# Kernel tuning notes

Measured on AMD Instinct MI355X. Metric: run time of the kernel, lower is better.

Reference implementation:

```python
import jax, jax.numpy as jnp
import numpy as np

B, S, HIDDEN = 2, 2048, 2048
HQ, HKV, D = 16, 4, 128
EPS = 1e-6
SCALE = D ** -0.5


def _deinterleave(x):
    # [..., D] interleaved pairs -> [x0,x2,...,x1,x3,...] (half layout)
    *lead, d = x.shape
    return x.reshape(*lead, d // 2, 2).swapaxes(-1, -2).reshape(*lead, d)


def _interleave(x):
    # inverse of _deinterleave
    *lead, d = x.shape
    return x.reshape(*lead, 2, d // 2).swapaxes(-1, -2).reshape(*lead, d)


def _rotate_half(x):
    x1, x2 = jnp.split(x, 2, axis=-1)
    return jnp.concatenate([-x2, x1], axis=-1)


def _rmsnorm(x, w):
    var = jnp.mean(jnp.square(x), axis=-1, keepdims=True)
    return x * jax.lax.rsqrt(var + EPS) * w


def setup_inputs() -> dict:
    key = jax.random.key(0)
    k0, k1, k2, k3, k4 = jax.random.split(key, 5)
    hidden_states = jax.random.normal(k0, (B, S, HIDDEN), jnp.float32)
    cos = jax.random.uniform(k1, (S, D), jnp.float32, -1.0, 1.0)
    sin = jax.random.uniform(k2, (S, D), jnp.float32, -1.0, 1.0)
    qkv_w = jax.random.normal(k3, ((HQ + 2 * HKV) * D, HIDDEN), jnp.float32) * 0.02
    qk_norm_w = jnp.ones((D,), jnp.float32)
    o_w = jax.random.normal(k4, (HIDDEN, HQ * D), jnp.float32) * 0.02
    return {"hidden_states": hidden_states, "cos": cos, "sin": sin,
            "qkv_w": qkv_w, "qk_norm_w": qk_norm_w, "o_w": o_w}


def reference(hidden_states, cos, sin, qkv_w, qk_norm_w, o_w):
    b, s, _ = hidden_states.shape
    qkv = jnp.einsum('bsh,oh->bso', hidden_states, qkv_w)  # [B,S,(HQ+2HKV)*D]
    q = qkv[..., : HQ * D].reshape(b, s, HQ, D)
    k = qkv[..., HQ * D:(HQ + HKV) * D].reshape(b, s, HKV, D)
    v = qkv[..., (HQ + HKV) * D:].reshape(b, s, HKV, D)

    # interleaved-layout RoPE: deinterleave -> rotate-half RoPE -> re-interleave
    q, k = _deinterleave(q), _deinterleave(k)
    cs = cos[None, :, None, :]
    sn = sin[None, :, None, :]
    q = q * cs + _rotate_half(q) * sn
    k = k * cs + _rotate_half(k) * sn
    q, k = _interleave(q), _interleave(k)

    # QK RMSNorm (shared weight over head_dim)
    q = _rmsnorm(q, qk_norm_w)
    k = _rmsnorm(k, qk_norm_w)

    # causal GQA attention
    g = HQ // HKV
    qg = q.reshape(b, s, HKV, g, D)
    scores = jnp.einsum('bshgd,bthd->bhgst', qg, k) * SCALE  # [B,HKV,g,S,S]
    causal = jnp.tril(jnp.ones((s, s), bool))
    scores = jnp.where(causal, scores, jnp.finfo(scores.dtype).min)
    probs = jax.nn.softmax(scores, axis=-1)
    attn = jnp.einsum('bhgst,bthd->bshgd', probs, v).reshape(b, s, HQ * D)

    return jnp.einsum('bsd,od->bso', attn, o_w)
```

## Files before the change

### kernel.cpp

```cpp
#include <hip/hip_runtime.h>
#include <hip/hip_bf16.h>

typedef __bf16 bf16_t;
typedef bf16_t bf16x8 __attribute__((ext_vector_type(8)));
typedef float f32x4 __attribute__((ext_vector_type(4)));
typedef float f32x16 __attribute__((ext_vector_type(16)));
typedef unsigned short u16;
typedef unsigned int u32;

#define B_    2
#define S_    2048
#define HID   2048
#define NQKV  3072
#define HQ_   16
#define HKV_  4
#define D_    128
#define QSCALE_ 0.12751879526600565f

__device__ __forceinline__ u16 f2b(float f) {
    __hip_bfloat16 h = __float2bfloat16(f);
    return *reinterpret_cast<u16*>(&h);
}

__global__ __launch_bounds__(256) void cvt_f32_bf16(const float* __restrict__ in,
                                                    u16* __restrict__ out, int n4) {
    int i = blockIdx.x * 256 + threadIdx.x;
    if (i >= n4) return;
    float4 v = reinterpret_cast<const float4*>(in)[i];
    ushort4 o;
    o.x = f2b(v.x); o.y = f2b(v.y); o.z = f2b(v.z); o.w = f2b(v.w);
    reinterpret_cast<ushort4*>(out)[i] = o;
}

__global__ __launch_bounds__(512, 1) void gemm256_bt(const u16* __restrict__ A,
                                                     const u16* __restrict__ Bm,
                                                     float* __restrict__ C,
                                                     int M, int N, int K) {
    extern __shared__ __align__(16) char smem[];
    u16* Asm = (u16*)smem;
    u16* Bsm = (u16*)smem + 32768;

    const int tid  = threadIdx.x;
    const int lane = tid & 63;
    const int wid  = tid >> 6;
    const int wr = wid >> 2, wc = wid & 3;
    const int lrow = lane & 15, lgrp = lane >> 4;
    const int swz  = (lrow & 7) << 4;
    const int m0 = blockIdx.x * 256, n0 = blockIdx.y * 256;

    const int stRow = tid >> 3;
    const int stCol = ((((tid & 7) * 16) ^ ((stRow & 7) << 4)) >> 1);

    const u16* aBase = A  + (size_t)(m0 + stRow) * K + stCol;
    const u16* bBase = Bm + (size_t)(n0 + stRow) * K + stCol;

    auto glds = [&](const u16* g, u16* l) {
        __builtin_amdgcn_global_load_lds(
            (const __attribute__((address_space(1))) void*)g,
            (__attribute__((address_space(3))) void*)l, 16, 0, 0);
    };
    auto stageA = [&](int buf, int h, int k0) {
        const u16* g = aBase + (size_t)(128 * h) * K + k0;
        u16* d = Asm + buf * 16384 + (1024 * h + tid) * 8;
        glds(g, d);
        glds(g + (size_t)64 * K, d + 512 * 8);
    };
    auto stageB = [&](int buf, int h, int k0) {
        const u16* g = bBase + (size_t)(128 * h) * K + k0;
        u16* d = Bsm + buf * 16384 + (1024 * h + tid) * 8;
        glds(g, d);
        glds(g + (size_t)64 * K, d + 512 * 8);
    };

    f32x4 acc[8][4] = {};
    const int KT = K >> 6;

    stageA(0, 0, 0); stageA(0, 1, 0); stageB(0, 0, 0); stageB(0, 1, 0);

    for (int x = 0; x < KT; ++x) {
        const int cur = x & 1;
        const int kn  = (x + 1) << 6;
        const bool pf = (x + 1 < KT);
        const char* aT = (const char*)(Asm + cur * 16384);
        const char* bT = (const char*)(Bsm + cur * 16384);

        auto ldA = [&](int mi, int ks) -> bf16x8 {
            int row = wr * 128 + mi * 16 + lrow;
            return *(const bf16x8*)(aT + row * 128 + ((ks * 64 + lgrp * 16) ^ swz));
        };
        auto ldB = [&](int ni, int ks) -> bf16x8 {
            int row = wc * 64 + ni * 16 + lrow;
            return *(const bf16x8*)(bT + row * 128 + ((ks * 64 + lgrp * 16) ^ swz));
        };

        bf16x8 afr[4][2], bfr[2][2];

        if (pf) {
            stageA(cur ^ 1, 0, kn);
            asm volatile("s_waitcnt vmcnt(2)" ::: "memory");
        } else {
            asm volatile("s_waitcnt vmcnt(0)" ::: "memory");
        }
        __builtin_amdgcn_s_barrier();
        #pragma unroll
        for (int mi = 0; mi < 4; ++mi) { afr[mi][0] = ldA(mi, 0); afr[mi][1] = ldA(mi, 1); }
        #pragma unroll
        for (int ni = 0; ni < 2; ++ni) { bfr[ni][0] = ldB(ni, 0); bfr[ni][1] = ldB(ni, 1); }
        __builtin_amdgcn_s_setprio(1);
        #pragma unroll
        for (int mi = 0; mi < 4; ++mi)
            #pragma unroll
            for (int ni = 0; ni < 2; ++ni) {
                acc[mi][ni] = __builtin_amdgcn_mfma_f32_16x16x32_bf16(afr[mi][0], bfr[ni][0], acc[mi][ni], 0, 0, 0);
                acc[mi][ni] = __builtin_amdgcn_mfma_f32_16x16x32_bf16(afr[mi][1], bfr[ni][1], acc[mi][ni], 0, 0, 0);
            }
        __builtin_amdgcn_s_setprio(0);
        __builtin_amdgcn_s_barrier();

        #pragma unroll
        for (int ni = 0; ni < 2; ++ni) { bfr[ni][0] = ldB(ni + 2, 0); bfr[ni][1] = ldB(ni + 2, 1); }
        if (pf) stageA(cur ^ 1, 1, kn);
        __builtin_amdgcn_s_barrier();
        __builtin_amdgcn_s_setprio(1);
        #pragma unroll
        for (int mi = 0; mi < 4; ++mi)
            #pragma unroll
            for (int ni = 0; ni < 2; ++ni) {
                acc[mi][ni + 2] = __builtin_amdgcn_mfma_f32_16x16x32_bf16(afr[mi][0], bfr[ni][0], acc[mi][ni + 2], 0, 0, 0);
                acc[mi][ni + 2] = __builtin_amdgcn_mfma_f32_16x16x32_bf16(afr[mi][1], bfr[ni][1], acc[mi][ni + 2], 0, 0, 0);
            }
        __builtin_amdgcn_s_setprio(0);
        __builtin_amdgcn_s_barrier();

        #pragma unroll
        for (int mi = 0; mi < 4; ++mi) { afr[mi][0] = ldA(mi + 4, 0); afr[mi][1] = ldA(mi + 4, 1); }
        if (pf) stageB(cur ^ 1, 0, kn);
        __builtin_amdgcn_s_barrier();
        __builtin_amdgcn_s_setprio(1);
        #pragma unroll
        for (int mi = 0; mi < 4; ++mi)
            #pragma unroll
            for (int ni = 0; ni < 2; ++ni) {
                acc[mi + 4][ni + 2] = __builtin_amdgcn_mfma_f32_16x16x32_bf16(afr[mi][0], bfr[ni][0], acc[mi + 4][ni + 2], 0, 0, 0);
                acc[mi + 4][ni + 2] = __builtin_amdgcn_mfma_f32_16x16x32_bf16(afr[mi][1], bfr[ni][1], acc[mi + 4][ni + 2], 0, 0, 0);
            }
        __builtin_amdgcn_s_setprio(0);
        __builtin_amdgcn_s_barrier();

        #pragma unroll
        for (int ni = 0; ni < 2; ++ni) { bfr[ni][0] = ldB(ni, 0); bfr[ni][1] = ldB(ni, 1); }
        if (pf) stageB(cur ^ 1, 1, kn);
        __builtin_amdgcn_s_barrier();
        __builtin_amdgcn_s_setprio(1);
        #pragma unroll
        for (int mi = 0; mi < 4; ++mi)
            #pragma unroll
            for (int ni = 0; ni < 2; ++ni) {
                acc[mi + 4][ni] = __builtin_amdgcn_mfma_f32_16x16x32_bf16(afr[mi][0], bfr[ni][0], acc[mi + 4][ni], 0, 0, 0);
                acc[mi + 4][ni] = __builtin_amdgcn_mfma_f32_16x16x32_bf16(afr[mi][1], bfr[ni][1], acc[mi + 4][ni], 0, 0, 0);
            }
        __builtin_amdgcn_s_setprio(0);
        __builtin_amdgcn_s_barrier();
    }

    #pragma unroll
    for (int mi = 0; mi < 8; ++mi)
        #pragma unroll
        for (int ni = 0; ni < 4; ++ni) {
            int r = m0 + wr * 128 + mi * 16 + lgrp * 4;
            int c = n0 + wc * 64 + ni * 16 + lrow;
            float* p = C + (size_t)r * N + c;
            #pragma unroll
            for (int i = 0; i < 4; ++i) p[(size_t)i * N] = acc[mi][ni][i];
        }
}

__global__ __launch_bounds__(256) void rope_norm_split(const float* __restrict__ qkv,
                                                       const float* __restrict__ cosb,
                                                       const float* __restrict__ sinb,
                                                       const float* __restrict__ nw,
                                                       u16* __restrict__ qb,
                                                       u16* __restrict__ kb,
                                                       u16* __restrict__ vb) {
    const int row  = blockIdx.x;
    const int b    = row >> 11;
    const int s    = row & 2047;
    const int wave = threadIdx.x >> 6;
    const int lane = threadIdx.x & 63;
    const float* base = qkv + (size_t)row * NQKV;

    const float c0 = cosb[s * 128 + lane];
    const float c1 = cosb[s * 128 + 64 + lane];
    const float s0 = sinb[s * 128 + lane];
    const float s1 = sinb[s * 128 + 64 + lane];
    const float w0 = nw[2 * lane];
    const float w1 = nw[2 * lane + 1];

    for (int h = wave; h < HQ_ + HKV_; h += 4) {
        float2 x = *(const float2*)(base + h * 128 + 2 * lane);
        float y0 = x.x * c0 - x.y * s0;
        float y1 = x.y * c1 + x.x * s1;
        float ss = y0 * y0 + y1 * y1;
        #pragma unroll
        for (int off = 32; off; off >>= 1) ss += __shfl_xor(ss, off);
        float r = rsqrtf(ss * (1.0f / 128.0f) + 1e-6f);
        float o0 = y0 * r * w0, o1 = y1 * r * w1;
        if (h < HQ_) {
            u32 pack = (u32)f2b(o0 * QSCALE_) | ((u32)f2b(o1 * QSCALE_) << 16);
            *(u32*)(qb + ((size_t)(b * HQ_ + h) * S_ + s) * D_ + 2 * lane) = pack;
        } else {
            u32 pack = (u32)f2b(o0) | ((u32)f2b(o1) << 16);
            *(u32*)(kb + ((size_t)(b * HKV_ + (h - HQ_)) * S_ + s) * D_ + 2 * lane) = pack;
        }
    }
    {
        int h = wave;
        float2 x = *(const float2*)(base + (HQ_ + HKV_) * 128 + h * 128 + 2 * lane);
        u32 pack = (u32)f2b(x.x) | ((u32)f2b(x.y) << 16);
        *(u32*)(vb + ((size_t)(b * HKV_ + h) * S_ + s) * D_ + 2 * lane) = pack;
    }
}

__global__ __launch_bounds__(256) void transpose_v(const u16* __restrict__ vb,
                                                   u16* __restrict__ vtb) {
    __shared__ u16 t[64][72];
    const int s0 = blockIdx.x * 64, d0 = blockIdx.y * 64, bh = blockIdx.z;
    const u16* src = vb  + (size_t)bh * S_ * D_;
    u16*       dst = vtb + (size_t)bh * D_ * S_;
    const int tid = threadIdx.x;

    {
        int r = tid >> 3, c8 = (tid & 7) * 8;
        #pragma unroll
        for (int p = 0; p < 2; p++) {
            int rr = r + p * 32;
            *(uint4*)&t[rr][c8] = *(const uint4*)(src + (size_t)(s0 + rr) * D_ + d0 + c8);
        }
    }
    __syncthreads();
    {
        int dd = tid & 63;
        int sb = (tid >> 6) * 8;
        #pragma unroll
        for (int p = 0; p < 2; p++) {
            int ss8 = sb + p * 32;
            union { u16 u[8]; uint4 v; } pk;
            #pragma unroll
            for (int j = 0; j < 8; j++) pk.u[j] = t[ss8 + j][dd];
            *(uint4*)(dst + (size_t)(d0 + dd) * S_ + s0 + ss8) = pk.v;
        }
    }
}

__global__ __launch_bounds__(256, 2) void attn_fwd3(const u16* __restrict__ qb,
                                                    const u16* __restrict__ kb,
                                                    const u16* __restrict__ vtb,
                                                    u16* __restrict__ attn) {
    __shared__ __align__(16) u16 Ks[2][64 * 128];
    __shared__ __align__(16) u16 Vs[2][128 * 64];

    const int bh  = blockIdx.y;
    const int qt  = (bh < 16) ? (15 - (int)blockIdx.x) : (int)blockIdx.x;
    const int b   = bh >> 4, hq = bh & 15, hkv = hq >> 2;
    const int tid = threadIdx.x;
    const int wave = tid >> 6, lane = tid & 63;
    const int l31 = lane & 31, hi = lane >> 5;
    const int swz = (l31 & 7) << 4;

    const u16* Q  = qb  + (size_t)(b * HQ_  + hq ) * S_ * D_;
    const u16* Kp = kb  + (size_t)(b * HKV_ + hkv) * S_ * D_;
    const u16* Vt = vtb + (size_t)(b * HKV_ + hkv) * D_ * S_;
    const int q0w = qt * 128 + wave * 32;
    const int qg  = q0w + l31;

    int kSrc[4], vSrc[4], cLds[4];
    #pragma unroll
    for (int p = 0; p < 4; p++) {
        int c = tid + p * 256;
        int kr = c >> 4, kc = ((c & 15) * 16) ^ ((kr & 7) << 4);
        kSrc[p] = kr * D_ + (kc >> 1);
        int vr = c >> 3, vc = ((c & 7) * 16) ^ ((vr & 7) << 4);
        vSrc[p] = vr * S_ + (vc >> 1);
        cLds[p] = c * 16;
    }

    auto STAGE = [&](int buf, int kv0s) {
        const u16* kbase = Kp + (size_t)kv0s * D_;
        const u16* vbase = Vt + kv0s;
        #pragma unroll
        for (int p = 0; p < 4; p++)
            __builtin_amdgcn_global_load_lds(
                (const __attribute__((address_space(1))) void*)(kbase + kSrc[p]),
                (__attribute__((address_space(3))) void*)((char*)Ks[buf] + cLds[p]), 16, 0, 0);
        #pragma unroll
        for (int p = 0; p < 4; p++)
            __builtin_amdgcn_global_load_lds(
                (const __attribute__((address_space(1))) void*)(vbase + vSrc[p]),
                (__attribute__((address_space(3))) void*)((char*)Vs[buf] + cLds[p]), 16, 0, 0);
    };

    bf16x8 qf[8];
    #pragma unroll
    for (int ds = 0; ds < 8; ds++)
        qf[ds] = *(const bf16x8*)(Q + (size_t)qg * D_ + ds * 16 + hi * 8);

    float m_run = -1e30f, l_run = 0.f;
    f32x16 oacc[4] = {};

    const int nkt = 2 * qt + 2;
    STAGE(0, 0);

    for (int kt = 0; kt < nkt; kt++) {
        const int cur = kt & 1;
        const int kv0 = kt * 64;
        if (kt + 1 < nkt) {
            STAGE(cur ^ 1, kv0 + 64);
            asm volatile("s_waitcnt vmcnt(8)" ::: "memory");
        } else {
            asm volatile("s_waitcnt vmcnt(0)" ::: "memory");
        }
        __builtin_amdgcn_s_barrier();

        const char* ksb = (const char*)Ks[cur];
        f32x16 sc[2] = {};
        __builtin_amdgcn_s_setprio(1);
        #pragma unroll
        for (int blk = 0; blk < 2; blk++) {
            const char* rowb = ksb + (blk * 32 + l31) * 256;
            #pragma unroll
            for (int ds = 0; ds < 8; ds++) {
                bf16x8 kf = *(const bf16x8*)(rowb + ((ds * 32 + hi * 16) ^ swz));
                sc[blk] = __builtin_amdgcn_mfma_f32_32x32x16_bf16(kf, qf[ds], sc[blk], 0, 0, 0);
            }
        }
        __builtin_amdgcn_s_setprio(0);

        if (kv0 + 63 > q0w) {
            #pragma unroll
            for (int blk = 0; blk < 2; blk++)
                #pragma unroll
                for (int r = 0; r < 16; r++) {
                    int kvg = kv0 + blk * 32 + (r & 3) + 8 * (r >> 2) + 4 * hi;
                    if (kvg > qg) sc[blk][r] = -1e30f;
                }
        }

        float t16[16];
        #pragma unroll
        for (int r = 0; r < 16; r++) t16[r] = fmaxf(sc[0][r], sc[1][r]);
        #pragma unroll
        for (int r = 0; r < 8; r++) t16[r] = fmaxf(t16[r], t16[r + 8]);
        #pragma unroll
        for (int r = 0; r < 4; r++) t16[r] = fmaxf(t16[r], t16[r + 4]);
        float mt = fmaxf(fmaxf(t16[0], t16[1]), fmaxf(t16[2], t16[3]));
        mt = fmaxf(mt, __shfl_xor(mt, 32));

        bool noDefer = !__all(mt <= m_run + 8.0f);
        float mnew = m_run;
        if (noDefer) {
            mnew = fmaxf(m_run, mt);
            float alpha = __builtin_amdgcn_exp2f(m_run - mnew);
            l_run *= alpha;
            #pragma unroll
            for (int d4 = 0; d4 < 4; d4++)
                #pragma unroll
                for (int r = 0; r < 16; r++) oacc[d4][r] *= alpha;
            m_run = mnew;
        }

        float la = 0.f;
        u32 pk0[8], pk1[8];
        #pragma unroll
        for (int g = 0; g < 4; g++)
            #pragma unroll
            for (int e = 0; e < 2; e++) {
                float a0 = __builtin_amdgcn_exp2f(sc[0][g * 4 + 2 * e]     - mnew);
                float b0 = __builtin_amdgcn_exp2f(sc[0][g * 4 + 2 * e + 1] - mnew);
                float a1 = __builtin_amdgcn_exp2f(sc[1][g * 4 + 2 * e]     - mnew);
                float b1 = __builtin_amdgcn_exp2f(sc[1][g * 4 + 2 * e + 1] - mnew);
                la += (a0 + b0) + (a1 + b1);
                pk0[g * 2 + e] = (u32)f2b(a0) | ((u32)f2b(b0) << 16);
                pk1[g * 2 + e] = (u32)f2b(a1) | ((u32)f2b(b1) << 16);
            }
        la += __shfl_xor(la, 32);
        l_run += la;

        u32 qk0[8], qk1[8];
        #pragma unroll
        for (int i = 0; i < 8; i++) {
            qk0[i] = __shfl_xor(pk0[i], 32);
            qk1[i] = __shfl_xor(pk1[i], 32);
        }

        const char* vsb = (const char*)Vs[cur];
        #pragma unroll
        for (int ks = 0; ks < 4; ks++) {
            const int i0 = (ks & 1) * 4;
            union { u32 w[4]; bf16x8 v; } pf;
            if (ks & 2) {
                pf.w[0] = hi ? qk1[i0 + 2] : pk1[i0 + 0];
                pf.w[1] = hi ? qk1[i0 + 3] : pk1[i0 + 1];
                pf.w[2] = hi ? pk1[i0 + 2] : qk1[i0 + 0];
                pf.w[3] = hi ? pk1[i0 + 3] : qk1[i0 + 1];
            } else {
                pf.w[0] = hi ? qk0[i0 + 2] : pk0[i0 + 0];
                pf.w[1] = hi ? qk0[i0 + 3] : pk0[i0 + 1];
                pf.w[2] = hi ? pk0[i0 + 2] : qk0[i0 + 0];
                pf.w[3] = hi ? pk0[i0 + 3] : qk0[i0 + 1];
            }
            __builtin_amdgcn_s_setprio(1);
            #pragma unroll
            for (int d4 = 0; d4 < 4; d4++) {
                bf16x8 vf = *(const bf16x8*)(vsb + (d4 * 32 + l31) * 128
                                                 + ((ks * 32 + hi * 16) ^ swz));
                oacc[d4] = __builtin_amdgcn_mfma_f32_32x32x16_bf16(vf, pf.v, oacc[d4], 0, 0, 0);
            }
            __builtin_amdgcn_s_setprio(0);
        }
        __builtin_amdgcn_s_barrier();
    }

    const float inv = 1.0f / l_run;
    u16* sl = (u16*)Ks + wave * (32 * 128);
    #pragma unroll
    for (int d4 = 0; d4 < 4; d4++)
        #pragma unroll
        for (int rp = 0; rp < 8; rp++) {
            int dbyte = d4 * 64 + 16 * (rp >> 1) + 8 * hi + 4 * (rp & 1);
            u32 w = (u32)f2b(oacc[d4][rp * 2] * inv)
                  | ((u32)f2b(oacc[d4][rp * 2 + 1] * inv) << 16);
            *(u32*)((char*)sl + l31 * 256 + (dbyte ^ swz)) = w;
        }
    #pragma unroll
    for (int j = 0; j < 8; j++) {
        int c = lane + j * 64;
        int qL = c >> 4, dc = c & 15;
        uint4 v = *(uint4*)((char*)sl + qL * 256 + ((dc * 16) ^ ((qL & 7) << 4)));
        int qrow = qt * 128 + wave * 32 + qL;
        *(uint4*)(attn + (size_t)(b * S_ + qrow) * (HQ_ * D_) + hq * D_ + dc * 8) = v;
    }
}

extern "C" void kernel_launch(void* const* d_in, const int* in_sizes, int n_in,
                              void* d_out, int out_size, void* d_ws, size_t ws_size,
                              hipStream_t stream) {
    const float* hidden = (const float*)d_in[0];
    const float* cosb   = (const float*)d_in[1];
    const float* sinb   = (const float*)d_in[2];
    const float* qkvw   = (const float*)d_in[3];
    const float* nw     = (const float*)d_in[4];
    const float* ow     = (const float*)d_in[5];
    float* out = (float*)d_out;

    const size_t M  = (size_t)B_ * S_;
    char* ws = (char*)d_ws;
    size_t off = 0;
    u16*   hb    = (u16*)(ws + off); off += M * HID * 2;
    u16*   wqkvb = (u16*)(ws + off); off += (size_t)NQKV * HID * 2;
    u16*   wob   = (u16*)(ws + off); off += (size_t)HID * (HQ_ * D_) * 2;
    float* qkv   = (float*)(ws + off); off += M * NQKV * 4;
    u16*   qb2   = (u16*)(ws + off); off += (size_t)B_ * HQ_  * S_ * D_ * 2;
    u16*   kb2   = (u16*)(ws + off); off += (size_t)B_ * HKV_ * S_ * D_ * 2;
    u16*   vb2   = (u16*)(ws + off); off += (size_t)B_ * HKV_ * S_ * D_ * 2;
    u16*   vtb   = (u16*)(ws + off); off += (size_t)B_ * HKV_ * S_ * D_ * 2;
    u16*   attn  = hb;

    {
        int n4 = (int)(M * HID / 4);
        cvt_f32_bf16<<<(n4 + 255) / 256, 256, 0, stream>>>(hidden, hb, n4);
    }
    {
        int n4 = NQKV * HID / 4;
        cvt_f32_bf16<<<(n4 + 255) / 256, 256, 0, stream>>>(qkvw, wqkvb, n4);
    }
    {
        int n4 = HID * (HQ_ * D_) / 4;
        cvt_f32_bf16<<<(n4 + 255) / 256, 256, 0, stream>>>(ow, wob, n4);
    }

    const int smemSz = 131072;
    hipFuncSetAttribute(reinterpret_cast<const void*>(gemm256_bt),
                        hipFuncAttributeMaxDynamicSharedMemorySize, smemSz);

    gemm256_bt<<<dim3(M / 256, NQKV / 256), 512, smemSz, stream>>>(hb, wqkvb, qkv,
                                                                   (int)M, NQKV, HID);

    rope_norm_split<<<(int)M, 256, 0, stream>>>(qkv, cosb, sinb, nw, qb2, kb2, vb2);

    transpose_v<<<dim3(S_ / 64, D_ / 64, B_ * HKV_), 256, 0, stream>>>(vb2, vtb);

    attn_fwd3<<<dim3(16, B_ * HQ_), 256, 0, stream>>>(qb2, kb2, vtb, attn);

    gemm256_bt<<<dim3(M / 256, HID / 256), 512, smemSz, stream>>>(attn, wob, out,
                                                                  (int)M, HID, HQ_ * D_);
}
```

Measured before the change: 232.9 us.

## Restructure GEMM prefetch waits and preload K/V fragments into registers in attention

In the GEMM, the first stage of the next tile's A load is now issued after the current fragments are read, and each iteration ends with a full vmcnt(0) wait rather than a partial wait at its start. The prologue now waits for all staged loads and adds a barrier. In the attention kernel, all K and V fragments for the tile are read from LDS into registers right after the score MFMAs. The end-of-iteration barrier moves to just after these reads, so the next prefetch can overwrite the buffer while softmax and PV still run. This costs many more VGPRs (vf alone is 16 bf16x8 registers) and may lower occupancy. The full vmcnt(0) wait in the GEMM may also expose global load latency.

```diff
diff --git a/kernel.cpp b/kernel.cpp
--- a/kernel.cpp
+++ b/kernel.cpp
@@ -76,6 +76,8 @@
     const int KT = K >> 6;
 
     stageA(0, 0, 0); stageA(0, 1, 0); stageB(0, 0, 0); stageB(0, 1, 0);
+    asm volatile("s_waitcnt vmcnt(0)" ::: "memory");
+    __builtin_amdgcn_s_barrier();
 
     for (int x = 0; x < KT; ++x) {
         const int cur = x & 1;
@@ -93,32 +95,27 @@
             return *(const bf16x8*)(bT + row * 128 + ((ks * 64 + lgrp * 16) ^ swz));
         };
 
-        bf16x8 afr[4][2], bfr[2][2];
-
-        if (pf) {
-            stageA(cur ^ 1, 0, kn);
-            asm volatile("s_waitcnt vmcnt(2)" ::: "memory");
-        } else {
-            asm volatile("s_waitcnt vmcnt(0)" ::: "memory");
-        }
-        __builtin_amdgcn_s_barrier();
-        #pragma unroll
-        for (int mi = 0; mi < 4; ++mi) { afr[mi][0] = ldA(mi, 0); afr[mi][1] = ldA(mi, 1); }
-        #pragma unroll
-        for (int ni = 0; ni < 2; ++ni) { bfr[ni][0] = ldB(ni, 0); bfr[ni][1] = ldB(ni, 1); }
+        bf16x8 a[4][2], b[2][2], b2[2][2];
+
+        #pragma unroll
+        for (int mi = 0; mi < 4; ++mi) { a[mi][0] = ldA(mi, 0); a[mi][1] = ldA(mi, 1); }
+        #pragma unroll
+        for (int ni = 0; ni < 2; ++ni) { b[ni][0] = ldB(ni, 0); b[ni][1] = ldB(ni, 1); }
+        if (pf) stageA(cur ^ 1, 0, kn);
+        __builtin_amdgcn_s_barrier();
         __builtin_amdgcn_s_setprio(1);
         #pragma unroll
         for (int mi = 0; mi < 4; ++mi)
             #pragma unroll
             for (int ni = 0; ni < 2; ++ni) {
-                acc[mi][ni] = __builtin_amdgcn_mfma_f32_16x16x32_bf16(afr[mi][0], bfr[ni][0], acc[mi][ni], 0, 0, 0);
-                acc[mi][ni] = __builtin_amdgcn_mfma_f32_16x16x32_bf16(afr[mi][1], bfr[ni][1], acc[mi][ni], 0, 0, 0);
+                acc[mi][ni] = __builtin_amdgcn_mfma_f32_16x16x32_bf16(a[mi][0], b[ni][0], acc[mi][ni], 0, 0, 0);
+                acc[mi][ni] = __builtin_amdgcn_mfma_f32_16x16x32_bf16(a[mi][1], b[ni][1], acc[mi][ni], 0, 0, 0);
             }
         __builtin_amdgcn_s_setprio(0);
         __builtin_amdgcn_s_barrier();
 
         #pragma unroll
-        for (int ni = 0; ni < 2; ++ni) { bfr[ni][0] = ldB(ni + 2, 0); bfr[ni][1] = ldB(ni + 2, 1); }
+        for (int ni = 0; ni < 2; ++ni) { b2[ni][0] = ldB(ni + 2, 0); b2[ni][1] = ldB(ni + 2, 1); }
         if (pf) stageA(cur ^ 1, 1, kn);
         __builtin_amdgcn_s_barrier();
         __builtin_amdgcn_s_setprio(1);
@@ -126,14 +123,14 @@
         for (int mi = 0; mi < 4; ++mi)
             #pragma unroll
             for (int ni = 0; ni < 2; ++ni) {
-                acc[mi][ni + 2] = __builtin_amdgcn_mfma_f32_16x16x32_bf16(afr[mi][0], bfr[ni][0], acc[mi][ni + 2], 0, 0, 0);
-                acc[mi][ni + 2] = __builtin_amdgcn_mfma_f32_16x16x32_bf16(afr[mi][1], bfr[ni][1], acc[mi][ni + 2], 0, 0, 0);
+                acc[mi][ni + 2] = __builtin_amdgcn_mfma_f32_16x16x32_bf16(a[mi][0], b2[ni][0], acc[mi][ni + 2], 0, 0, 0);
+                acc[mi][ni + 2] = __builtin_amdgcn_mfma_f32_16x16x32_bf16(a[mi][1], b2[ni][1], acc[mi][ni + 2], 0, 0, 0);
             }
         __builtin_amdgcn_s_setprio(0);
         __builtin_amdgcn_s_barrier();
 
         #pragma unroll
-        for (int mi = 0; mi < 4; ++mi) { afr[mi][0] = ldA(mi + 4, 0); afr[mi][1] = ldA(mi + 4, 1); }
+        for (int mi = 0; mi < 4; ++mi) { a[mi][0] = ldA(mi + 4, 0); a[mi][1] = ldA(mi + 4, 1); }
         if (pf) stageB(cur ^ 1, 0, kn);
         __builtin_amdgcn_s_barrier();
         __builtin_amdgcn_s_setprio(1);
@@ -141,14 +138,14 @@
         for (int mi = 0; mi < 4; ++mi)
             #pragma unroll
             for (int ni = 0; ni < 2; ++ni) {
-                acc[mi + 4][ni + 2] = __builtin_amdgcn_mfma_f32_16x16x32_bf16(afr[mi][0], bfr[ni][0], acc[mi + 4][ni + 2], 0, 0, 0);
-                acc[mi + 4][ni + 2] = __builtin_amdgcn_mfma_f32_16x16x32_bf16(afr[mi][1], bfr[ni][1], acc[mi + 4][ni + 2], 0, 0, 0);
+                acc[mi + 4][ni + 2] = __builtin_amdgcn_mfma_f32_16x16x32_bf16(a[mi][0], b2[ni][0], acc[mi + 4][ni + 2], 0, 0, 0);
+                acc[mi + 4][ni + 2] = __builtin_amdgcn_mfma_f32_16x16x32_bf16(a[mi][1], b2[ni][1], acc[mi + 4][ni + 2], 0, 0, 0);
             }
         __builtin_amdgcn_s_setprio(0);
         __builtin_amdgcn_s_barrier();
 
         #pragma unroll
-        for (int ni = 0; ni < 2; ++ni) { bfr[ni][0] = ldB(ni, 0); bfr[ni][1] = ldB(ni, 1); }
+        for (int ni = 0; ni < 2; ++ni) { b[ni][0] = ldB(ni, 0); b[ni][1] = ldB(ni, 1); }
         if (pf) stageB(cur ^ 1, 1, kn);
         __builtin_amdgcn_s_barrier();
         __builtin_amdgcn_s_setprio(1);
@@ -156,10 +153,11 @@
         for (int mi = 0; mi < 4; ++mi)
             #pragma unroll
             for (int ni = 0; ni < 2; ++ni) {
-                acc[mi + 4][ni] = __builtin_amdgcn_mfma_f32_16x16x32_bf16(afr[mi][0], bfr[ni][0], acc[mi + 4][ni], 0, 0, 0);
-                acc[mi + 4][ni] = __builtin_amdgcn_mfma_f32_16x16x32_bf16(afr[mi][1], bfr[ni][1], acc[mi + 4][ni], 0, 0, 0);
+                acc[mi + 4][ni] = __builtin_amdgcn_mfma_f32_16x16x32_bf16(a[mi][0], b[ni][0], acc[mi + 4][ni], 0, 0, 0);
+                acc[mi + 4][ni] = __builtin_amdgcn_mfma_f32_16x16x32_bf16(a[mi][1], b[ni][1], acc[mi + 4][ni], 0, 0, 0);
             }
         __builtin_amdgcn_s_setprio(0);
+        asm volatile("s_waitcnt vmcnt(0)" ::: "memory");
         __builtin_amdgcn_s_barrier();
     }
 
@@ -322,18 +320,33 @@
         __builtin_amdgcn_s_barrier();
 
         const char* ksb = (const char*)Ks[cur];
+        const char* vsb = (const char*)Vs[cur];
+        const char* rb0 = ksb + l31 * 256;
+        const char* rb1 = rb0 + 32 * 256;
+        bf16x8 kA[8], kB[8];
+        #pragma unroll
+        for (int ds = 0; ds < 8; ds++) kA[ds] = *(const bf16x8*)(rb0 + ((ds * 32 + hi * 16) ^ swz));
+        #pragma unroll
+        for (int ds = 0; ds < 8; ds++) kB[ds] = *(const bf16x8*)(rb1 + ((ds * 32 + hi * 16) ^ swz));
+
         f32x16 sc[2] = {};
         __builtin_amdgcn_s_setprio(1);
         #pragma unroll
-        for (int blk = 0; blk < 2; blk++) {
-            const char* rowb = ksb + (blk * 32 + l31) * 256;
-            #pragma unroll
-            for (int ds = 0; ds < 8; ds++) {
-                bf16x8 kf = *(const bf16x8*)(rowb + ((ds * 32 + hi * 16) ^ swz));
-                sc[blk] = __builtin_amdgcn_mfma_f32_32x32x16_bf16(kf, qf[ds], sc[blk], 0, 0, 0);
-            }
-        }
+        for (int ds = 0; ds < 8; ds++)
+            sc[0] = __builtin_amdgcn_mfma_f32_32x32x16_bf16(kA[ds], qf[ds], sc[0], 0, 0, 0);
+        #pragma unroll
+        for (int ds = 0; ds < 8; ds++)
+            sc[1] = __builtin_amdgcn_mfma_f32_32x32x16_bf16(kB[ds], qf[ds], sc[1], 0, 0, 0);
         __builtin_amdgcn_s_setprio(0);
+
+        bf16x8 vf[4][4];
+        #pragma unroll
+        for (int ks = 0; ks < 4; ks++)
+            #pragma unroll
+            for (int d4 = 0; d4 < 4; d4++)
+                vf[ks][d4] = *(const bf16x8*)(vsb + (d4 * 32 + l31) * 128
+                                                  + ((ks * 32 + hi * 16) ^ swz));
+        __builtin_amdgcn_s_barrier();
 
         if (kv0 + 63 > q0w) {
             #pragma unroll
@@ -392,32 +405,27 @@
             qk1[i] = __shfl_xor(pk1[i], 32);
         }
 
-        const char* vsb = (const char*)Vs[cur];
         #pragma unroll
         for (int ks = 0; ks < 4; ks++) {
             const int i0 = (ks & 1) * 4;
-            union { u32 w[4]; bf16x8 v; } pf;
+            union { u32 w[4]; bf16x8 v; } pfv;
             if (ks & 2) {
-                pf.w[0] = hi ? qk1[i0 + 2] : pk1[i0 + 0];
-                pf.w[1] = hi ? qk1[i0 + 3] : pk1[i0 + 1];
-                pf.w[2] = hi ? pk1[i0 + 2] : qk1[i0 + 0];
-                pf.w[3] = hi ? pk1[i0 + 3] : qk1[i0 + 1];
+                pfv.w[0] = hi ? qk1[i0 + 2] : pk1[i0 + 0];
+                pfv.w[1] = hi ? qk1[i0 + 3] : pk1[i0 + 1];
+                pfv.w[2] = hi ? pk1[i0 + 2] : qk1[i0 + 0];
+                pfv.w[3] = hi ? pk1[i0 + 3] : qk1[i0 + 1];
             } else {
-                pf.w[0] = hi ? qk0[i0 + 2] : pk0[i0 + 0];
-                pf.w[1] = hi ? qk0[i0 + 3] : pk0[i0 + 1];
-                pf.w[2] = hi ? pk0[i0 + 2] : qk0[i0 + 0];
-                pf.w[3] = hi ? pk0[i0 + 3] : qk0[i0 + 1];
+                pfv.w[0] = hi ? qk0[i0 + 2] : pk0[i0 + 0];
+                pfv.w[1] = hi ? qk0[i0 + 3] : pk0[i0 + 1];
+                pfv.w[2] = hi ? pk0[i0 + 2] : qk0[i0 + 0];
+                pfv.w[3] = hi ? pk0[i0 + 3] : qk0[i0 + 1];
             }
             __builtin_amdgcn_s_setprio(1);
             #pragma unroll
-            for (int d4 = 0; d4 < 4; d4++) {
-                bf16x8 vf = *(const bf16x8*)(vsb + (d4 * 32 + l31) * 128
-                                                 + ((ks * 32 + hi * 16) ^ swz));
-                oacc[d4] = __builtin_amdgcn_mfma_f32_32x32x16_bf16(vf, pf.v, oacc[d4], 0, 0, 0);
-            }
+            for (int d4 = 0; d4 < 4; d4++)
+                oacc[d4] = __builtin_amdgcn_mfma_f32_32x32x16_bf16(vf[ks][d4], pfv.v, oacc[d4], 0, 0, 0);
             __builtin_amdgcn_s_setprio(0);
         }
-        __builtin_amdgcn_s_barrier();
     }
 
     const float inv = 1.0f / l_run;
```

Result: no change. 234.2 us (+0.6%).
